# Kernel tuning notes

Hardware: AMD Instinct MI355X
Metric: run time of the kernel (lower is better)

The kernel has to match this reference:

```python
import jax, jax.numpy as jnp
import numpy as np

B, S, D, H = 2, 2048, 128, 8
HD = D // H  # 16


def setup_inputs() -> dict:
    key = jax.random.key(0)
    ks = jax.random.split(key, 12)
    rnd = lambda k, sh, sc=1.0: jax.random.normal(k, sh, dtype=jnp.float32) * sc
    uni = lambda k, sh: jax.random.uniform(k, sh, dtype=jnp.float32) * 0.1  # scaled to keep softmax unsaturated
    return dict(
        x_tgt=rnd(ks[0], (B, S, D)),
        enc_out=rnd(ks[1], (B, S, D)),
        self_wq=uni(ks[2], (D, D)),
        self_wk=uni(ks[3], (D, D)),
        self_wv=uni(ks[4], (D, D)),
        cross_wq=uni(ks[5], (D, D)),
        cross_wk=uni(ks[6], (D, D)),
        cross_wv=uni(ks[7], (D, D)),
        w1=rnd(ks[8], (D, D), 0.02), b1=jnp.zeros((D,), jnp.float32),
        w2=rnd(ks[9], (D, D), 0.02), b2=jnp.zeros((D,), jnp.float32),
        w3=rnd(ks[10], (D, 4 * D), 0.02), b3=jnp.zeros((4 * D,), jnp.float32),
        w4=rnd(ks[11], (4 * D, D), 0.02), b4=jnp.zeros((D,), jnp.float32),
        mask_src=jnp.ones((B, S), jnp.int32),
        mask_tgt=jnp.ones((B, S), jnp.int32),
    )


def _split(t):
    # faithful to torch: reshape (B,S,HD,H) then permute -> (B,H,S,HD)
    b, s, _ = t.shape
    return jnp.transpose(t.reshape(b, s, HD, H), (0, 3, 1, 2))


def _merge(t):
    # inverse: (B,H,S,HD) -> (B,S,HD,H) -> (B,S,D)
    b, _, s, _ = t.shape
    return jnp.transpose(t, (0, 2, 3, 1)).reshape(b, s, D)


def _attn(x_kv, x_q, wq, wk, wv):
    q = _split(x_q @ wq)   # (B,H,Sq,HD)
    k = _split(x_kv @ wk)  # (B,H,Sk,HD)
    v = _split(x_kv @ wv)
    scores = jnp.einsum('bhqd,bhkd->bhqk', q, k) / jnp.sqrt(jnp.float32(HD))
    p = jax.nn.softmax(scores, axis=-1)  # masked=True branch: no additive mask
    return _merge(jnp.einsum('bhqk,bhkd->bhqd', p, v))


def _layer_norm(x):
    # eps-less custom norm: (x - mean) / var, with unbiased variance (N-1)
    m = jnp.mean(x, axis=-1, keepdims=True)
    c = x - m
    var = jnp.sum(c * c, axis=-1, keepdims=True) / (D - 1)
    return c / var


def reference(x_tgt, enc_out, self_wq, self_wk, self_wv, cross_wq, cross_wk, cross_wv,
              w1, b1, w2, b2, w3, b3, w4, b4, mask_src, mask_tgt):
    # masked self-attention on target embeddings (no causal mask in source code)
    sa = _attn(x_tgt, x_tgt, self_wq, self_wk, self_wv)
    r1 = sa @ w1 + b1 + x_tgt
    # 'cross' attention: K/V from decoder input, Q from encoder output (faithful quirk)
    ca = _attn(x_tgt, enc_out, cross_wq, cross_wk, cross_wv)
    r2 = ca @ w2 + b2 + r1
    ln = _layer_norm(r2)
    h = jax.nn.relu(ln @ w3 + b3)
    return h @ w4 + b4 + r2
```

## Files before the change

kernel.cpp:

```cpp
#include <hip/hip_runtime.h>
#include <hip/hip_bf16.h>

#define BB 2
#define SS 2048
#define DD 128
#define HH 8
#define HDIM 16
#define DF 512
#define SPK 36
#define HS 520
#define LNS 136

typedef float floatx4 __attribute__((ext_vector_type(4)));
typedef float floatx16 __attribute__((ext_vector_type(16)));
typedef short frag8 __attribute__((ext_vector_type(8)));

__device__ __forceinline__ short f2bf(float x) {
  union { __hip_bfloat16 h; short s; } u;
  u.h = __float2bfloat16(x);
  return u.s;
}
__device__ __forceinline__ unsigned int pkbf(float a, float b) {
  float2 f; f.x = a; f.y = b;
  union { __hip_bfloat162 h2; unsigned int u; } u;
  u.h2 = __float22bfloat162_rn(f);
  return u.u;
}
__device__ __forceinline__ frag8 cvt8(const float4 a, const float4 b) {
  union { frag8 f; unsigned int u[4]; } x;
  x.u[0] = pkbf(a.x, a.y);
  x.u[1] = pkbf(a.z, a.w);
  x.u[2] = pkbf(b.x, b.y);
  x.u[3] = pkbf(b.z, b.w);
  return x.f;
}

struct WSrc { const float* p[10]; };
__global__ __launch_bounds__(256) void wprep_kernel(WSrc w, short* __restrict__ dst) {
  const int wi = blockIdx.y;
  const int kshift = (wi == 9) ? 9 : 7;
  const int N = (wi == 8) ? 512 : 128;
  const int total = N << kshift;
  const int offs[10] = {0, 16384, 32768, 49152, 65536, 81920, 98304, 114688, 131072, 196608};
  const float sc = (wi == 0 || wi == 3) ? 0.25f * 1.4426950408889634f : 1.0f;
  const float* src = w.p[wi];
  short* d = dst + offs[wi];
  const int K = 1 << kshift;
  for (int idx = blockIdx.x * 256 + threadIdx.x; idx < total; idx += gridDim.x * 256) {
    const int n = idx >> kshift, k = idx & (K - 1);
    d[idx] = f2bf(src[k * N + n] * sc);
  }
}

__global__ __launch_bounds__(128) void qkv_kernel(const float* __restrict__ x_tgt,
                                                  const float* __restrict__ enc_out,
                                                  const short* __restrict__ wt,
                                                  short* __restrict__ Qs, short* __restrict__ Ks,
                                                  short* __restrict__ Vts,
                                                  short* __restrict__ Qc, short* __restrict__ Kc,
                                                  short* __restrict__ Vtc) {
  const int t = threadIdx.x, wv = t >> 6, lane = t & 63;
  const int quad = lane >> 4, l16 = lane & 15;
  const int mbase = blockIdx.x * 16;
  const int which = blockIdx.y;
  const int kind = which % 3;
  const float* A = (which == 3) ? enc_out : x_tgt;
  const short* W = wt + which * 16384;
  short* Qb = (which < 3) ? Qs : Qc;
  short* Kb = (which < 3) ? Ks : Kc;
  short* Vtb = (which < 3) ? Vts : Vtc;

  __shared__ short sC[16 * 130];

  floatx4 acc[4];
#pragma unroll
  for (int ci = 0; ci < 4; ci++) acc[ci] = (floatx4){0.f, 0.f, 0.f, 0.f};

#pragma unroll
  for (int ks = 0; ks < 4; ks++) {
    const float4* ar = (const float4*)&A[(size_t)(mbase + l16) * DD + ks * 32 + quad * 8];
    const frag8 af = cvt8(ar[0], ar[1]);
#pragma unroll
    for (int ci = 0; ci < 4; ci++) {
      const int ct = wv * 4 + ci;
      const frag8 bf = *(const frag8*)&W[(ct * 16 + l16) * DD + ks * 32 + quad * 8];
      acc[ci] = __builtin_amdgcn_mfma_f32_16x16x32_bf16(af, bf, acc[ci], 0, 0, 0);
    }
  }

#pragma unroll
  for (int ci = 0; ci < 4; ci++) {
#pragma unroll
    for (int r = 0; r < 4; r++) {
      sC[(quad * 4 + r) * 130 + (wv * 4 + ci) * 16 + l16] = f2bf(acc[ci][r]);
    }
  }
  __syncthreads();

  const int b = mbase >> 11;
  const int sbase = mbase & 2047;
  if (kind <= 1) {
    short* Dst = (kind == 0) ? Qb : Kb;
    const int s = lane >> 2, c4 = lane & 3;
#pragma unroll
    for (int hh = 0; hh < 4; hh++) {
      const int h = wv * 4 + hh;
      short4 v;
      v.x = sC[s * 130 + (c4 * 4 + 0) * 8 + h];
      v.y = sC[s * 130 + (c4 * 4 + 1) * 8 + h];
      v.z = sC[s * 130 + (c4 * 4 + 2) * 8 + h];
      v.w = sC[s * 130 + (c4 * 4 + 3) * 8 + h];
      const int bh = b * HH + h;
      *(short4*)&Dst[((size_t)bh * SS + sbase + s) * HDIM + c4 * 4] = v;
    }
  } else {
    const int dci = lane >> 2, c4 = lane & 3;
#pragma unroll
    for (int hh = 0; hh < 4; hh++) {
      const int h = wv * 4 + hh;
      short4 v;
      v.x = sC[(c4 * 4 + 0) * 130 + dci * 8 + h];
      v.y = sC[(c4 * 4 + 1) * 130 + dci * 8 + h];
      v.z = sC[(c4 * 4 + 2) * 130 + dci * 8 + h];
      v.w = sC[(c4 * 4 + 3) * 130 + dci * 8 + h];
      const int bh = b * HH + h;
      *(short4*)&Vtb[((size_t)bh * HDIM + dci) * SS + sbase + c4 * 4] = v;
    }
  }
}

__global__ __launch_bounds__(256) void attn_mfma_kernel(
    const short* __restrict__ Qa, const short* __restrict__ Ka,
    const short* __restrict__ Vta, short* __restrict__ AMa,
    const short* __restrict__ Qc, const short* __restrict__ Kc,
    const short* __restrict__ Vtc, short* __restrict__ AMc) {
  const int t = threadIdx.x, wid = t >> 6, lane = t & 63;
  const int l32 = lane & 31, half = lane >> 5;
  const int quad = (lane >> 4) & 3, l16 = lane & 15;
  const int bh = blockIdx.y;
  const int qbase = blockIdx.x * 32;
  const int inst = blockIdx.z;
  const short* Q = inst ? Qc : Qa;
  const short* K = inst ? Kc : Ka;
  const short* Vt = inst ? Vtc : Vta;
  short* AM = inst ? AMc : AMa;
  const size_t headoff = (size_t)bh * SS;

  __shared__ short sP[2][4][32 * SPK];

  const frag8 qf = *(const frag8*)&Q[(headoff + qbase + l32) * HDIM + half * 8];

  frag8 onef;
#pragma unroll
  for (int i = 0; i < 8; i++) onef[i] = (short)0x3f80;

  floatx4 acc_o[2], acc_l[2];
  acc_o[0] = (floatx4){0.f, 0.f, 0.f, 0.f}; acc_o[1] = acc_o[0];
  acc_l[0] = acc_o[0]; acc_l[1] = acc_o[0];

  const int keyw = wid * 512;
#pragma unroll 2
  for (int it = 0; it < 16; it++) {
    const int kb = keyw + it * 32;
    short* sPw = &sP[it & 1][wid][0];
    const frag8 kf = *(const frag8*)&K[(headoff + kb + l32) * HDIM + half * 8];
    const floatx16 z16 = {0.f};
    const floatx16 sc = __builtin_amdgcn_mfma_f32_32x32x16_bf16(kf, qf, z16, 0, 0, 0);
#pragma unroll
    for (int g = 0; g < 4; g++) {
      const float e0 = __builtin_amdgcn_exp2f(sc[4 * g + 0]);
      const float e1 = __builtin_amdgcn_exp2f(sc[4 * g + 1]);
      const float e2 = __builtin_amdgcn_exp2f(sc[4 * g + 2]);
      const float e3 = __builtin_amdgcn_exp2f(sc[4 * g + 3]);
      uint2 pk;
      pk.x = pkbf(e0, e1);
      pk.y = pkbf(e2, e3);
      *(uint2*)&sPw[l32 * SPK + g * 8 + half * 4] = pk;
    }
#pragma unroll
    for (int qh = 0; qh < 2; qh++) {
      const frag8 pf = *(const frag8*)&sPw[(qh * 16 + l16) * SPK + quad * 8];
      const frag8 vf = *(const frag8*)&Vt[((size_t)bh * HDIM + l16) * SS + kb + quad * 8];
      acc_o[qh] = __builtin_amdgcn_mfma_f32_16x16x32_bf16(vf, pf, acc_o[qh], 0, 0, 0);
      acc_l[qh] = __builtin_amdgcn_mfma_f32_16x16x32_bf16(onef, pf, acc_l[qh], 0, 0, 0);
    }
  }

  {
    float* pn = (float*)&sP[0][wid][0];
    float* plw = (float*)&sP[1][wid][0];
#pragma unroll
    for (int qh = 0; qh < 2; qh++) {
#pragma unroll
      for (int r = 0; r < 4; r++) {
        pn[(quad * 4 + r) * 33 + qh * 16 + l16] = acc_o[qh][r];
      }
      if (quad == 0) plw[qh * 16 + l16] = acc_l[qh][0];
    }
  }
  __syncthreads();

  {
    const int b = bh >> 3, h = bh & 7;
#pragma unroll
    for (int idx = t; idx < 512; idx += 256) {
      const int q16 = idx & 31, d = idx >> 5;
      float num = 0.f, l = 0.f;
#pragma unroll
      for (int w = 0; w < 4; w++) {
        num += ((const float*)&sP[0][w][0])[d * 33 + q16];
        l += ((const float*)&sP[1][w][0])[q16];
      }
      AM[((size_t)b * SS + qbase + q16) * DD + d * 8 + h] = f2bf(num / l);
    }
  }
}

__global__ __launch_bounds__(512) void tail_kernel(
    const short* __restrict__ AMs, const short* __restrict__ AMc,
    const short* __restrict__ W1, const short* __restrict__ W2,
    const float* __restrict__ b1, const float* __restrict__ b2,
    const float* __restrict__ x_tgt,
    const short* __restrict__ W3, const float* __restrict__ b3,
    const short* __restrict__ W4, const float* __restrict__ b4,
    float* __restrict__ Out) {
  const int t = threadIdx.x, w = t >> 6, lane = t & 63;
  const int quad = lane >> 4, l16 = lane & 15;
  const int mbase = blockIdx.x * 16;
  const int nA = w * 16 + l16;

  __shared__ float sumS[8][16];
  __shared__ float sumQ[8][16];
  __shared__ short sLN[16 * LNS];
  __shared__ short hs[16 * HS];

  floatx4 acc2 = (floatx4){0.f, 0.f, 0.f, 0.f};
#pragma unroll
  for (int ks = 0; ks < 4; ks++) {
    const frag8 afS = *(const frag8*)&AMs[(size_t)(mbase + l16) * DD + ks * 32 + quad * 8];
    const frag8 afC = *(const frag8*)&AMc[(size_t)(mbase + l16) * DD + ks * 32 + quad * 8];
    const frag8 bf1 = *(const frag8*)&W1[nA * DD + ks * 32 + quad * 8];
    const frag8 bf2 = *(const frag8*)&W2[nA * DD + ks * 32 + quad * 8];
    acc2 = __builtin_amdgcn_mfma_f32_16x16x32_bf16(afS, bf1, acc2, 0, 0, 0);
    acc2 = __builtin_amdgcn_mfma_f32_16x16x32_bf16(afC, bf2, acc2, 0, 0, 0);
  }

  float v[4];
  {
    const float bn = b1[nA] + b2[nA];
#pragma unroll
    for (int r = 0; r < 4; r++) {
      const int m = mbase + quad * 4 + r;
      v[r] = acc2[r] + bn + x_tgt[(size_t)m * DD + nA];
    }
  }

#pragma unroll
  for (int r = 0; r < 4; r++) {
    float s = v[r];
    float sq = v[r] * v[r];
#pragma unroll
    for (int mk = 1; mk < 16; mk <<= 1) {
      s += __shfl_xor(s, mk, 64);
      sq += __shfl_xor(sq, mk, 64);
    }
    if (l16 == 0) {
      sumS[w][quad * 4 + r] = s;
      sumQ[w][quad * 4 + r] = sq;
    }
  }
  __syncthreads();

#pragma unroll
  for (int r = 0; r < 4; r++) {
    const int row = quad * 4 + r;
    float S = 0.f, Qs_ = 0.f;
#pragma unroll
    for (int ww = 0; ww < 8; ww++) { S += sumS[ww][row]; Qs_ += sumQ[ww][row]; }
    const float mean = S * (1.0f / 128.0f);
    const float cs = Qs_ - S * mean;
    const float ivar = 127.0f / cs;
    sLN[row * LNS + nA] = f2bf((v[r] - mean) * ivar);
  }
  __syncthreads();

  {
    floatx4 acc[4];
#pragma unroll
    for (int ci = 0; ci < 4; ci++) acc[ci] = (floatx4){0.f, 0.f, 0.f, 0.f};
    const int nblk = w * 64;
#pragma unroll
    for (int ks = 0; ks < 4; ks++) {
      const frag8 af = *(const frag8*)&sLN[l16 * LNS + ks * 32 + quad * 8];
#pragma unroll
      for (int ci = 0; ci < 4; ci++) {
        const frag8 bf = *(const frag8*)&W3[(size_t)(nblk + ci * 16 + l16) * DD + ks * 32 + quad * 8];
        acc[ci] = __builtin_amdgcn_mfma_f32_16x16x32_bf16(af, bf, acc[ci], 0, 0, 0);
      }
    }
#pragma unroll
    for (int ci = 0; ci < 4; ci++) {
      const int n = nblk + ci * 16 + l16;
      const float bn = b3[n];
#pragma unroll
      for (int r = 0; r < 4; r++) {
        hs[(quad * 4 + r) * HS + n] = f2bf(fmaxf(acc[ci][r] + bn, 0.f));
      }
    }
  }
  __syncthreads();

  {
    floatx4 acc = (floatx4){0.f, 0.f, 0.f, 0.f};
#pragma unroll 4
    for (int ks = 0; ks < 16; ks++) {
      const frag8 af = *(const frag8*)&hs[l16 * HS + ks * 32 + quad * 8];
      const frag8 bf = *(const frag8*)&W4[(size_t)nA * DF + ks * 32 + quad * 8];
      acc = __builtin_amdgcn_mfma_f32_16x16x32_bf16(af, bf, acc, 0, 0, 0);
    }
    const float bn = b4[nA];
#pragma unroll
    for (int r = 0; r < 4; r++) {
      const int m = mbase + quad * 4 + r;
      Out[(size_t)m * DD + nA] = acc[r] + bn + v[r];
    }
  }
}

extern "C" void kernel_launch(void* const* d_in, const int* in_sizes, int n_in,
                              void* d_out, int out_size, void* d_ws, size_t ws_size,
                              hipStream_t stream) {
  (void)in_sizes; (void)n_in; (void)out_size; (void)ws_size;
  const float* x_tgt   = (const float*)d_in[0];
  const float* enc_out = (const float*)d_in[1];
  const float* b1 = (const float*)d_in[9];
  const float* b2 = (const float*)d_in[11];
  const float* b3 = (const float*)d_in[13];
  const float* b4 = (const float*)d_in[15];

  WSrc wsrc;
  wsrc.p[0] = (const float*)d_in[2];
  wsrc.p[1] = (const float*)d_in[3];
  wsrc.p[2] = (const float*)d_in[4];
  wsrc.p[3] = (const float*)d_in[5];
  wsrc.p[4] = (const float*)d_in[6];
  wsrc.p[5] = (const float*)d_in[7];
  wsrc.p[6] = (const float*)d_in[8];
  wsrc.p[7] = (const float*)d_in[10];
  wsrc.p[8] = (const float*)d_in[12];
  wsrc.p[9] = (const float*)d_in[14];

  float* ws = (float*)d_ws;
  short* wt   = (short*)(ws + 0);
  short* Qs   = (short*)(ws + 131072);
  short* Ks   = (short*)(ws + 393216);
  short* Vts  = (short*)(ws + 655360);
  short* AMs  = (short*)(ws + 917504);
  short* Qc   = (short*)(ws + 1179648);
  short* Kc   = (short*)(ws + 1441792);
  short* Vtc  = (short*)(ws + 1703936);
  short* AMc  = (short*)(ws + 1966080);

  const int M = BB * SS;
  const int MT = M / 16;

  wprep_kernel<<<dim3(64, 10), 256, 0, stream>>>(wsrc, wt);

  qkv_kernel<<<dim3(MT, 6), 128, 0, stream>>>(x_tgt, enc_out, wt, Qs, Ks, Vts, Qc, Kc, Vtc);

  attn_mfma_kernel<<<dim3(SS / 32, BB * HH, 2), 256, 0, stream>>>(
      Qs, Ks, Vts, AMs, Qc, Kc, Vtc, AMc);

  tail_kernel<<<MT, 512, 0, stream>>>(AMs, AMc, wt + 98304, wt + 114688,
                                      b1, b2, x_tgt, wt + 131072, b3,
                                      wt + 196608, b4, (float*)d_out);
}
```

Before: 156.9 us.

## Keep softmax probabilities in registers and fold row-sum into a 32x32 PV MFMA

The attention kernel no longer writes exp'd scores to shared memory and reads them back for separate PV and row-sum MFMAs. Instead it reshuffles the score accumulator between half-waves with a cross-lane shuffle to form the A operand and runs one 32x32x16 MFMA per 16 keys against a V^T padded to 32 rows, where row 16 holds ones so the softmax denominator comes out of the same MFMA. The workspace is re-laid out to hold the padded V^T, and the ones row is filled by an extra slice of the weight-prep kernel. In exchange this adds shuffles, extra V^T memory and wasted MFMA columns (rows 17-31 are unused), and the loop unroll drops to 1.

```diff
diff --git a/kernel.cpp b/kernel.cpp
--- a/kernel.cpp
+++ b/kernel.cpp
@@ -7,7 +7,6 @@
 #define HH 8
 #define HDIM 16
 #define DF 512
-#define SPK 36
 #define HS 520
 #define LNS 136
 
@@ -36,8 +35,21 @@
 }
 
 struct WSrc { const float* p[10]; };
-__global__ __launch_bounds__(256) void wprep_kernel(WSrc w, short* __restrict__ dst) {
+__global__ __launch_bounds__(256) void wprep_kernel(WSrc w, short* __restrict__ dst,
+                                                    short* __restrict__ Vts,
+                                                    short* __restrict__ Vtc) {
   const int wi = blockIdx.y;
+  if (wi == 10) {
+    const int total = 2 * BB * HH * SS;
+    for (int idx = blockIdx.x * 256 + threadIdx.x; idx < total; idx += gridDim.x * 256) {
+      const int inst2 = idx >> 15;
+      const int rest = idx & 32767;
+      const int bh = rest >> 11, s = rest & 2047;
+      short* vt = inst2 ? Vtc : Vts;
+      vt[((size_t)bh * 32 + 16) * SS + s] = (short)0x3f80;
+    }
+    return;
+  }
   const int kshift = (wi == 9) ? 9 : 7;
   const int N = (wi == 8) ? 512 : 128;
   const int total = N << kshift;
@@ -124,7 +136,7 @@
       v.z = sC[(c4 * 4 + 2) * 130 + dci * 8 + h];
       v.w = sC[(c4 * 4 + 3) * 130 + dci * 8 + h];
       const int bh = b * HH + h;
-      *(short4*)&Vtb[((size_t)bh * HDIM + dci) * SS + sbase + c4 * 4] = v;
+      *(short4*)&Vtb[((size_t)bh * 32 + dci) * SS + sbase + c4 * 4] = v;
     }
   }
 }
@@ -136,7 +148,6 @@
     const short* __restrict__ Vtc, short* __restrict__ AMc) {
   const int t = threadIdx.x, wid = t >> 6, lane = t & 63;
   const int l32 = lane & 31, half = lane >> 5;
-  const int quad = (lane >> 4) & 3, l16 = lane & 15;
   const int bh = blockIdx.y;
   const int qbase = blockIdx.x * 32;
   const int inst = blockIdx.z;
@@ -145,57 +156,55 @@
   const short* Vt = inst ? Vtc : Vta;
   short* AM = inst ? AMc : AMa;
   const size_t headoff = (size_t)bh * SS;
-
-  __shared__ short sP[2][4][32 * SPK];
+  const bool hi = (half == 1);
+
+  __shared__ float pnum[4][32 * 16];
+  __shared__ float pl[4][32];
 
   const frag8 qf = *(const frag8*)&Q[(headoff + qbase + l32) * HDIM + half * 8];
 
-  frag8 onef;
-#pragma unroll
-  for (int i = 0; i < 8; i++) onef[i] = (short)0x3f80;
-
-  floatx4 acc_o[2], acc_l[2];
-  acc_o[0] = (floatx4){0.f, 0.f, 0.f, 0.f}; acc_o[1] = acc_o[0];
-  acc_l[0] = acc_o[0]; acc_l[1] = acc_o[0];
+  floatx16 acc = {0.f};
 
   const int keyw = wid * 512;
-#pragma unroll 2
+#pragma unroll 1
   for (int it = 0; it < 16; it++) {
     const int kb = keyw + it * 32;
-    short* sPw = &sP[it & 1][wid][0];
     const frag8 kf = *(const frag8*)&K[(headoff + kb + l32) * HDIM + half * 8];
     const floatx16 z16 = {0.f};
     const floatx16 sc = __builtin_amdgcn_mfma_f32_32x32x16_bf16(kf, qf, z16, 0, 0, 0);
-#pragma unroll
-    for (int g = 0; g < 4; g++) {
-      const float e0 = __builtin_amdgcn_exp2f(sc[4 * g + 0]);
-      const float e1 = __builtin_amdgcn_exp2f(sc[4 * g + 1]);
-      const float e2 = __builtin_amdgcn_exp2f(sc[4 * g + 2]);
-      const float e3 = __builtin_amdgcn_exp2f(sc[4 * g + 3]);
-      uint2 pk;
-      pk.x = pkbf(e0, e1);
-      pk.y = pkbf(e2, e3);
-      *(uint2*)&sPw[l32 * SPK + g * 8 + half * 4] = pk;
-    }
-#pragma unroll
-    for (int qh = 0; qh < 2; qh++) {
-      const frag8 pf = *(const frag8*)&sPw[(qh * 16 + l16) * SPK + quad * 8];
-      const frag8 vf = *(const frag8*)&Vt[((size_t)bh * HDIM + l16) * SS + kb + quad * 8];
-      acc_o[qh] = __builtin_amdgcn_mfma_f32_16x16x32_bf16(vf, pf, acc_o[qh], 0, 0, 0);
-      acc_l[qh] = __builtin_amdgcn_mfma_f32_16x16x32_bf16(onef, pf, acc_l[qh], 0, 0, 0);
-    }
-  }
-
-  {
-    float* pn = (float*)&sP[0][wid][0];
-    float* plw = (float*)&sP[1][wid][0];
-#pragma unroll
-    for (int qh = 0; qh < 2; qh++) {
-#pragma unroll
-      for (int r = 0; r < 4; r++) {
-        pn[(quad * 4 + r) * 33 + qh * 16 + l16] = acc_o[qh][r];
-      }
-      if (quad == 0) plw[qh * 16 + l16] = acc_l[qh][0];
+    unsigned ua[8];
+#pragma unroll
+    for (int p = 0; p < 8; p++) {
+      ua[p] = pkbf(__builtin_amdgcn_exp2f(sc[2 * p]),
+                   __builtin_amdgcn_exp2f(sc[2 * p + 1]));
+    }
+#pragma unroll
+    for (int c = 0; c < 2; c++) {
+      const unsigned s0 = hi ? ua[4 * c + 0] : ua[4 * c + 2];
+      const unsigned s1 = hi ? ua[4 * c + 1] : ua[4 * c + 3];
+      const unsigned y0 = __shfl_xor(s0, 32);
+      const unsigned y1 = __shfl_xor(s1, 32);
+      union { frag8 f; unsigned u[4]; } af;
+      af.u[0] = hi ? y0 : ua[4 * c + 0];
+      af.u[1] = hi ? y1 : ua[4 * c + 1];
+      af.u[2] = hi ? ua[4 * c + 2] : y0;
+      af.u[3] = hi ? ua[4 * c + 3] : y1;
+      const frag8 vf = *(const frag8*)&Vt[((size_t)bh * 32 + l32) * SS + kb + c * 16 + half * 8];
+      acc = __builtin_amdgcn_mfma_f32_32x32x16_bf16(af.f, vf, acc, 0, 0, 0);
+    }
+  }
+
+  if (l32 < 16) {
+#pragma unroll
+    for (int r = 0; r < 16; r++) {
+      const int q = (r & 3) + 8 * (r >> 2) + 4 * half;
+      pnum[wid][q * 16 + l32] = acc[r];
+    }
+  } else if (l32 == 16) {
+#pragma unroll
+    for (int r = 0; r < 16; r++) {
+      const int q = (r & 3) + 8 * (r >> 2) + 4 * half;
+      pl[wid][q] = acc[r];
     }
   }
   __syncthreads();
@@ -204,14 +213,14 @@
     const int b = bh >> 3, h = bh & 7;
 #pragma unroll
     for (int idx = t; idx < 512; idx += 256) {
-      const int q16 = idx & 31, d = idx >> 5;
+      const int d = idx & 15, q = idx >> 4;
       float num = 0.f, l = 0.f;
 #pragma unroll
       for (int w = 0; w < 4; w++) {
-        num += ((const float*)&sP[0][w][0])[d * 33 + q16];
-        l += ((const float*)&sP[1][w][0])[q16];
+        num += pnum[w][q * 16 + d];
+        l += pl[w][q];
       }
-      AM[((size_t)b * SS + qbase + q16) * DD + d * 8 + h] = f2bf(num / l);
+      AM[((size_t)b * SS + qbase + q) * DD + d * 8 + h] = f2bf(num / l);
     }
   }
 }
@@ -355,16 +364,16 @@
   short* Qs   = (short*)(ws + 131072);
   short* Ks   = (short*)(ws + 393216);
   short* Vts  = (short*)(ws + 655360);
-  short* AMs  = (short*)(ws + 917504);
-  short* Qc   = (short*)(ws + 1179648);
-  short* Kc   = (short*)(ws + 1441792);
-  short* Vtc  = (short*)(ws + 1703936);
-  short* AMc  = (short*)(ws + 1966080);
+  short* AMs  = (short*)(ws + 1179648);
+  short* Qc   = (short*)(ws + 1441792);
+  short* Kc   = (short*)(ws + 1703936);
+  short* Vtc  = (short*)(ws + 1966080);
+  short* AMc  = (short*)(ws + 2490368);
 
   const int M = BB * SS;
   const int MT = M / 16;
 
-  wprep_kernel<<<dim3(64, 10), 256, 0, stream>>>(wsrc, wt);
+  wprep_kernel<<<dim3(64, 11), 256, 0, stream>>>(wsrc, wt, Vts, Vtc);
 
   qkv_kernel<<<dim3(MT, 6), 128, 0, stream>>>(x_tgt, enc_out, wt, Qs, Ks, Vts, Qc, Kc, Vtc);
 
```

New measurement: 155.5 us. Within noise of the previous version (-0.9%).
